# Performance work log

Hardware: AMD Instinct MI355X
Metric: run time of the kernel (lower is better)

Reference implementation:

```python
import jax, jax.numpy as jnp
import numpy as np
from jax import lax

SEQ = 8192
H = 2048
DEPTH = 2


def _rnn_layer(xs, h0, Wih, Whh, bih, bhh):
    """Elman RNN layer. xs: (T, B, F); h0: (B, H). Returns (hs (T,B,H), hT (B,H)).
    h_t = tanh(x_t @ Wih^T + b_ih + h_{t-1} @ Whh^T + b_hh)  (PyTorch nn.RNN math)."""
    # Precompute the input projection for all steps at once (one big GEMM).
    x_proj = jnp.einsum('tbf,hf->tbh', xs, Wih) + bih  # (T, B, H)

    def step(h, xp):
        h_new = jnp.tanh(xp + h @ Whh.T + bhh)
        return h_new, h_new

    hT, hs = lax.scan(step, h0, x_proj)
    return hs, hT


def setup_inputs() -> dict:
    key = jax.random.key(0)
    ks = jax.random.split(key, 10)
    s = 1.0 / np.sqrt(H)  # PyTorch nn.RNN init scale (uniform +-1/sqrt(H)); use scaled normal
    return {
        'x': jax.random.normal(ks[0], (1, SEQ), jnp.float32),
        'h': jax.random.normal(ks[1], (DEPTH, 1, H), jnp.float32),
        'W_ih_0': jax.random.normal(ks[2], (H, 1), jnp.float32) * s,
        'W_hh_0': jax.random.normal(ks[3], (H, H), jnp.float32) * s,
        'b_ih_0': jax.random.normal(ks[4], (H,), jnp.float32) * s,
        'b_hh_0': jax.random.normal(ks[5], (H,), jnp.float32) * s,
        'W_ih_1': jax.random.normal(ks[6], (H, H), jnp.float32) * s,
        'W_hh_1': jax.random.normal(ks[7], (H, H), jnp.float32) * s,
        'b_ih_1': jax.random.normal(ks[8], (H,), jnp.float32) * s,
        'b_hh_1': jax.random.normal(ks[9], (H,), jnp.float32) * s,
    }


def reference(x, h, W_ih_0, W_hh_0, b_ih_0, b_hh_0, W_ih_1, W_hh_1, b_ih_1, b_hh_1):
    # x: (1, SEQ) -> x.t()[..., None] -> (SEQ, 1, 1)
    xs = x.T[..., None]
    layers = [
        (W_ih_0, W_hh_0, b_ih_0, b_hh_0),
        (W_ih_1, W_hh_1, b_ih_1, b_hh_1),
    ]
    finals = []
    for l, (Wih, Whh, bih, bhh) in enumerate(layers):
        xs, hT = _rnn_layer(xs, h[l], Wih, Whh, bih, bhh)
        finals.append(hT)
    return jnp.stack(finals)  # (DEPTH, 1, H) == h_n from nn.RNN
```

## Files before the change

### kernel.cpp

```cpp
#include <hip/hip_runtime.h>
#include <hip/hip_bf16.h>

#define HD 2048
#define TT 8192
#define RPB 8
#define NTHR 256
#define SENTU 0xAAAAAAAAu


__device__ __forceinline__ float fix_sent(float v) {
    return (__float_as_uint(v) == SENTU) ? __uint_as_float(0xAAAAAABAu) : v;
}
__device__ __forceinline__ void slot_store(float* p, float v) {
    __hip_atomic_store(p, fix_sent(v), __ATOMIC_RELAXED, __HIP_MEMORY_SCOPE_AGENT);
}
__device__ __forceinline__ unsigned long long slot_load64(const unsigned long long* p) {
    return __hip_atomic_load(p, __ATOMIC_RELAXED, __HIP_MEMORY_SCOPE_AGENT);
}

__device__ __forceinline__ void poll8(const float* src, float* stash, long& gbudget) {
    const unsigned long long* p = reinterpret_cast<const unsigned long long*>(src);
    unsigned long long v[4];
    bool got[4] = {false, false, false, false};
    int passes = 1024;
    for (;;) {
        bool ok = true;
        #pragma unroll
        for (int j = 0; j < 4; ++j) if (!got[j]) {
            unsigned long long t = slot_load64(p + j);
            if ((unsigned)t != SENTU && (unsigned)(t >> 32) != SENTU) { v[j] = t; got[j] = true; }
            else ok = false;
        }
        if (ok) break;
        if (--passes < 0 || --gbudget < 0) {
            #pragma unroll
            for (int j = 0; j < 4; ++j) if (!got[j]) v[j] = 0ull;
            break;
        }
        if (passes < 1016) __builtin_amdgcn_s_sleep(1);
    }
    #pragma unroll
    for (int j = 0; j < 4; ++j) {
        stash[2*j]   = __uint_as_float((unsigned)v[j]);
        stash[2*j+1] = __uint_as_float((unsigned)(v[j] >> 32));
    }
}

__device__ __forceinline__ void poll8x2(const float* srcA, const float* srcB,
                                        float* stA, float* stB, long& gbudget) {
    const unsigned long long* pA = reinterpret_cast<const unsigned long long*>(srcA);
    const unsigned long long* pB = reinterpret_cast<const unsigned long long*>(srcB);
    unsigned long long vA[4], vB[4];
    bool gA[4] = {false,false,false,false}, gB[4] = {false,false,false,false};
    int passes = 1024;
    for (;;) {
        bool ok = true;
        #pragma unroll
        for (int j = 0; j < 4; ++j) {
            if (!gA[j]) {
                unsigned long long t = slot_load64(pA + j);
                if ((unsigned)t != SENTU && (unsigned)(t >> 32) != SENTU) { vA[j] = t; gA[j] = true; }
                else ok = false;
            }
            if (!gB[j]) {
                unsigned long long t = slot_load64(pB + j);
                if ((unsigned)t != SENTU && (unsigned)(t >> 32) != SENTU) { vB[j] = t; gB[j] = true; }
                else ok = false;
            }
        }
        if (ok) break;
        if (--passes < 0 || --gbudget < 0) {
            #pragma unroll
            for (int j = 0; j < 4; ++j) { if (!gA[j]) vA[j] = 0ull; if (!gB[j]) vB[j] = 0ull; }
            break;
        }
        if (passes < 1016) __builtin_amdgcn_s_sleep(1);
    }
    #pragma unroll
    for (int j = 0; j < 4; ++j) {
        stA[2*j]   = __uint_as_float((unsigned)vA[j]);
        stA[2*j+1] = __uint_as_float((unsigned)(vA[j] >> 32));
        stB[2*j]   = __uint_as_float((unsigned)vB[j]);
        stB[2*j+1] = __uint_as_float((unsigned)(vB[j] >> 32));
    }
}

__global__ __launch_bounds__(NTHR, 2)
void rnn_fused(const float* __restrict__ x,
               const float* __restrict__ h_init,
               const float* __restrict__ Wih0,
               const float* __restrict__ Whh0,
               const float* __restrict__ bih0,
               const float* __restrict__ bhh0,
               const float* __restrict__ Wih1,
               const float* __restrict__ Whh1,
               const float* __restrict__ bih1,
               const float* __restrict__ bhh1,
               float* __restrict__ slots0,
               float* __restrict__ slots1,
               float* __restrict__ out)
{
    __shared__ float hbA[2][HD];
    __shared__ float hbB[2][HD];

    const int tid = threadIdx.x;
    const int bid = blockIdx.x;
    const bool l0 = (bid < 256);
    const int rb  = l0 ? bid : (bid - 256);
    const int r   = tid >> 5;
    const int l   = tid & 31;
    const int row = rb * RPB + r;

    const int swz_w = ((tid >> 3) & 7) << 2;
    const int swz_r = (l & 7) << 2;

    float lastv = 0.f;
    long  gbudget = 1L << 21;

    if (l0) {
        float w[64];
        {
            const float4* wr = reinterpret_cast<const float4*>(Whh0 + (size_t)row * HD + l * 64);
            #pragma unroll
            for (int j = 0; j < 16; ++j) {
                float4 v = wr[j];
                w[4*j+0] = v.x; w[4*j+1] = v.y; w[4*j+2] = v.z; w[4*j+3] = v.w;
            }
        }
        const float wx   = Wih0[row];
        const float bias = bih0[row] + bhh0[row];

        if (l == 0) slot_store(&slots0[row], h_init[row]);

        for (int s = 0; s < TT; ++s) {
            float stash[8];
            poll8(slots0 + (size_t)s * HD + tid * 8, stash, gbudget);

            float* hbuf = hbA[s & 1];
            {
                const int base = tid * 8;
                float4 v0 = make_float4(stash[0], stash[1], stash[2], stash[3]);
                float4 v1 = make_float4(stash[4], stash[5], stash[6], stash[7]);
                *reinterpret_cast<float4*>(&hbuf[(base    ) ^ swz_w]) = v0;
                *reinterpret_cast<float4*>(&hbuf[(base + 4) ^ swz_w]) = v1;
            }
            __syncthreads();

            float acc = 0.f;
            const int hbase = l * 64;
            #pragma unroll
            for (int q = 0; q < 16; ++q) {
                float4 hv = *reinterpret_cast<const float4*>(&hbuf[(hbase + 4*q) ^ swz_r]);
                acc = fmaf(w[4*q+0], hv.x, acc);
                acc = fmaf(w[4*q+1], hv.y, acc);
                acc = fmaf(w[4*q+2], hv.z, acc);
                acc = fmaf(w[4*q+3], hv.w, acc);
            }
            #pragma unroll
            for (int m = 1; m < 32; m <<= 1) acc += __shfl_xor(acc, m);

            float val = tanhf(acc + bias + x[s] * wx);
            lastv = val;
            if (l == 0) slot_store(&slots0[(size_t)(s + 1) * HD + row], val);
        }
        if (l == 0) out[row] = lastv;
    } else {
        float wh[64], wi[64];
        {
            const float4* a = reinterpret_cast<const float4*>(Whh1 + (size_t)row * HD + l * 64);
            const float4* b = reinterpret_cast<const float4*>(Wih1 + (size_t)row * HD + l * 64);
            #pragma unroll
            for (int j = 0; j < 16; ++j) {
                float4 v = a[j];
                wh[4*j+0] = v.x; wh[4*j+1] = v.y; wh[4*j+2] = v.z; wh[4*j+3] = v.w;
                float4 u = b[j];
                wi[4*j+0] = u.x; wi[4*j+1] = u.y; wi[4*j+2] = u.z; wi[4*j+3] = u.w;
            }
        }
        const float bias = bih1[row] + bhh1[row];

        if (l == 0) slot_store(&slots1[row], h_init[HD + row]);

        for (int s = 0; s < TT; ++s) {
            float st1[8], st0[8];
            poll8x2(slots1 + (size_t)s * HD + tid * 8,
                    slots0 + (size_t)(s + 1) * HD + tid * 8,
                    st1, st0, gbudget);

            float* b1 = hbA[s & 1];
            float* b0 = hbB[s & 1];
            {
                const int base = tid * 8;
                *reinterpret_cast<float4*>(&b1[(base    ) ^ swz_w]) = make_float4(st1[0], st1[1], st1[2], st1[3]);
                *reinterpret_cast<float4*>(&b1[(base + 4) ^ swz_w]) = make_float4(st1[4], st1[5], st1[6], st1[7]);
                *reinterpret_cast<float4*>(&b0[(base    ) ^ swz_w]) = make_float4(st0[0], st0[1], st0[2], st0[3]);
                *reinterpret_cast<float4*>(&b0[(base + 4) ^ swz_w]) = make_float4(st0[4], st0[5], st0[6], st0[7]);
            }
            __syncthreads();

            float acc = 0.f;
            const int hbase = l * 64;
            #pragma unroll
            for (int q = 0; q < 16; ++q) {
                float4 h1v = *reinterpret_cast<const float4*>(&b1[(hbase + 4*q) ^ swz_r]);
                float4 h0v = *reinterpret_cast<const float4*>(&b0[(hbase + 4*q) ^ swz_r]);
                acc = fmaf(wh[4*q+0], h1v.x, acc);
                acc = fmaf(wh[4*q+1], h1v.y, acc);
                acc = fmaf(wh[4*q+2], h1v.z, acc);
                acc = fmaf(wh[4*q+3], h1v.w, acc);
                acc = fmaf(wi[4*q+0], h0v.x, acc);
                acc = fmaf(wi[4*q+1], h0v.y, acc);
                acc = fmaf(wi[4*q+2], h0v.z, acc);
                acc = fmaf(wi[4*q+3], h0v.w, acc);
            }
            #pragma unroll
            for (int m = 1; m < 32; m <<= 1) acc += __shfl_xor(acc, m);

            float val = tanhf(acc + bias);
            lastv = val;
            if (l == 0) slot_store(&slots1[(size_t)(s + 1) * HD + row], val);
        }
        if (l == 0) out[HD + row] = lastv;
    }
}

extern "C" void kernel_launch(void* const* d_in, const int* in_sizes, int n_in,
                              void* d_out, int out_size, void* d_ws, size_t ws_size,
                              hipStream_t stream)
{
    const float* x    = (const float*)d_in[0];
    const float* h    = (const float*)d_in[1];
    const float* Wih0 = (const float*)d_in[2];
    const float* Whh0 = (const float*)d_in[3];
    const float* bih0 = (const float*)d_in[4];
    const float* bhh0 = (const float*)d_in[5];
    const float* Wih1 = (const float*)d_in[6];
    const float* Whh1 = (const float*)d_in[7];
    const float* bih1 = (const float*)d_in[8];
    const float* bhh1 = (const float*)d_in[9];
    float* out = (float*)d_out;

    float* slots0 = (float*)d_ws;
    float* slots1 = slots0 + (size_t)(TT + 1) * HD;
    size_t need = (size_t)2 * (TT + 1) * HD * sizeof(float);
    if (ws_size < need) return;

    hipMemsetAsync(d_ws, 0xAA, need, stream);

    hipLaunchKernelGGL(rnn_fused, dim3(512), dim3(NTHR), 0, stream,
                       x, h, Wih0, Whh0, bih0, bhh0, Wih1, Whh1, bih1, bhh1,
                       slots0, slots1, out);
}
```

Measured before the change: 46.70 ms.

## Double rows per block, halve block count, and publish hidden state as paired 64-bit stores

Each block now handles 16 rows with 512 threads, so only 256 blocks (128 per layer) take part in the per-step spin-wait handoff instead of 512. Each wavefront packs its two rows' outputs into one 64-bit atomic store, and each thread polls 4 floats instead of 8. The x[s] load is hoisted ahead of the poll. The aim is to cut the number of producers and consumers and the store traffic in the per-timestep global handoff. In exchange, each block has fewer threads per row for polling, and with launch_bounds(512,2) holding 128 weight registers per thread, register pressure could limit occupancy.

Result: faster. 40.59 ms (-13.1%).

```diff
diff --git a/kernel.cpp b/kernel.cpp
--- a/kernel.cpp
+++ b/kernel.cpp
@@ -3,86 +3,62 @@
 
 #define HD 2048
 #define TT 8192
-#define RPB 8
-#define NTHR 256
+#define RPB 16
+#define NTHR 512
 #define SENTU 0xAAAAAAAAu
 
 
-__device__ __forceinline__ float fix_sent(float v) {
-    return (__float_as_uint(v) == SENTU) ? __uint_as_float(0xAAAAAABAu) : v;
-}
-__device__ __forceinline__ void slot_store(float* p, float v) {
-    __hip_atomic_store(p, fix_sent(v), __ATOMIC_RELAXED, __HIP_MEMORY_SCOPE_AGENT);
-}
-__device__ __forceinline__ unsigned long long slot_load64(const unsigned long long* p) {
+typedef unsigned long long ull;
+
+__device__ __forceinline__ unsigned fix_sent_u(float v) {
+    unsigned u = __float_as_uint(v);
+    return (u == SENTU) ? 0xAAAAAABAu : u;
+}
+__device__ __forceinline__ void slot_store_pair(ull* p, float lo, float hi) {
+    ull v = (ull)fix_sent_u(lo) | ((ull)fix_sent_u(hi) << 32);
+    __hip_atomic_store(p, v, __ATOMIC_RELAXED, __HIP_MEMORY_SCOPE_AGENT);
+}
+__device__ __forceinline__ ull slot_load64(const ull* p) {
     return __hip_atomic_load(p, __ATOMIC_RELAXED, __HIP_MEMORY_SCOPE_AGENT);
 }
-
-__device__ __forceinline__ void poll8(const float* src, float* stash, long& gbudget) {
-    const unsigned long long* p = reinterpret_cast<const unsigned long long*>(src);
-    unsigned long long v[4];
-    bool got[4] = {false, false, false, false};
+__device__ __forceinline__ bool pair_ok(ull t) {
+    return ((unsigned)t != SENTU) && ((unsigned)(t >> 32) != SENTU);
+}
+
+__device__ __forceinline__ void poll2(const ull* p, ull v[2], long& gb) {
+    bool g0 = false, g1 = false;
     int passes = 1024;
     for (;;) {
-        bool ok = true;
-        #pragma unroll
-        for (int j = 0; j < 4; ++j) if (!got[j]) {
-            unsigned long long t = slot_load64(p + j);
-            if ((unsigned)t != SENTU && (unsigned)(t >> 32) != SENTU) { v[j] = t; got[j] = true; }
-            else ok = false;
-        }
-        if (ok) break;
-        if (--passes < 0 || --gbudget < 0) {
-            #pragma unroll
-            for (int j = 0; j < 4; ++j) if (!got[j]) v[j] = 0ull;
-            break;
-        }
+        if (!g0) { ull t = slot_load64(p);     if (pair_ok(t)) { v[0] = t; g0 = true; } }
+        if (!g1) { ull t = slot_load64(p + 1); if (pair_ok(t)) { v[1] = t; g1 = true; } }
+        if (g0 && g1) return;
+        if (--passes < 0 || --gb < 0) { if (!g0) v[0] = 0; if (!g1) v[1] = 0; return; }
         if (passes < 1016) __builtin_amdgcn_s_sleep(1);
     }
-    #pragma unroll
-    for (int j = 0; j < 4; ++j) {
-        stash[2*j]   = __uint_as_float((unsigned)v[j]);
-        stash[2*j+1] = __uint_as_float((unsigned)(v[j] >> 32));
-    }
-}
-
-__device__ __forceinline__ void poll8x2(const float* srcA, const float* srcB,
-                                        float* stA, float* stB, long& gbudget) {
-    const unsigned long long* pA = reinterpret_cast<const unsigned long long*>(srcA);
-    const unsigned long long* pB = reinterpret_cast<const unsigned long long*>(srcB);
-    unsigned long long vA[4], vB[4];
-    bool gA[4] = {false,false,false,false}, gB[4] = {false,false,false,false};
+}
+__device__ __forceinline__ void poll2x2(const ull* pA, const ull* pB,
+                                        ull vA[2], ull vB[2], long& gb) {
+    bool a0=false, a1=false, b0=false, b1=false;
     int passes = 1024;
     for (;;) {
-        bool ok = true;
-        #pragma unroll
-        for (int j = 0; j < 4; ++j) {
-            if (!gA[j]) {
-                unsigned long long t = slot_load64(pA + j);
-                if ((unsigned)t != SENTU && (unsigned)(t >> 32) != SENTU) { vA[j] = t; gA[j] = true; }
-                else ok = false;
-            }
-            if (!gB[j]) {
-                unsigned long long t = slot_load64(pB + j);
-                if ((unsigned)t != SENTU && (unsigned)(t >> 32) != SENTU) { vB[j] = t; gB[j] = true; }
-                else ok = false;
-            }
-        }
-        if (ok) break;
-        if (--passes < 0 || --gbudget < 0) {
-            #pragma unroll
-            for (int j = 0; j < 4; ++j) { if (!gA[j]) vA[j] = 0ull; if (!gB[j]) vB[j] = 0ull; }
-            break;
+        if (!a0) { ull t = slot_load64(pA);     if (pair_ok(t)) { vA[0] = t; a0 = true; } }
+        if (!a1) { ull t = slot_load64(pA + 1); if (pair_ok(t)) { vA[1] = t; a1 = true; } }
+        if (!b0) { ull t = slot_load64(pB);     if (pair_ok(t)) { vB[0] = t; b0 = true; } }
+        if (!b1) { ull t = slot_load64(pB + 1); if (pair_ok(t)) { vB[1] = t; b1 = true; } }
+        if (a0 && a1 && b0 && b1) return;
+        if (--passes < 0 || --gb < 0) {
+            if (!a0) vA[0] = 0; if (!a1) vA[1] = 0;
+            if (!b0) vB[0] = 0; if (!b1) vB[1] = 0;
+            return;
         }
         if (passes < 1016) __builtin_amdgcn_s_sleep(1);
     }
-    #pragma unroll
-    for (int j = 0; j < 4; ++j) {
-        stA[2*j]   = __uint_as_float((unsigned)vA[j]);
-        stA[2*j+1] = __uint_as_float((unsigned)(vA[j] >> 32));
-        stB[2*j]   = __uint_as_float((unsigned)vB[j]);
-        stB[2*j+1] = __uint_as_float((unsigned)(vB[j] >> 32));
-    }
+}
+__device__ __forceinline__ float4 unpack4(ull v0, ull v1) {
+    return make_float4(__uint_as_float((unsigned)v0),
+                       __uint_as_float((unsigned)(v0 >> 32)),
+                       __uint_as_float((unsigned)v1),
+                       __uint_as_float((unsigned)(v1 >> 32)));
 }
 
 __global__ __launch_bounds__(NTHR, 2)
@@ -105,19 +81,23 @@
 
     const int tid = threadIdx.x;
     const int bid = blockIdx.x;
-    const bool l0 = (bid < 256);
-    const int rb  = l0 ? bid : (bid - 256);
+    const bool is_l0 = (bid < 128);
+    const int blk = is_l0 ? bid : (bid - 128);
     const int r   = tid >> 5;
     const int l   = tid & 31;
-    const int row = rb * RPB + r;
-
-    const int swz_w = ((tid >> 3) & 7) << 2;
+    const int fl  = tid & 63;
+    const int wid = tid >> 6;
+    const int row = blk * RPB + r;
+
+    const int swz_w = ((tid >> 4) & 7) << 2;
     const int swz_r = (l & 7) << 2;
+
+    const size_t mypair_w = (size_t)blk * RPB + 2 * wid;
 
     float lastv = 0.f;
     long  gbudget = 1L << 21;
 
-    if (l0) {
+    if (is_l0) {
         float w[64];
         {
             const float4* wr = reinterpret_cast<const float4*>(Whh0 + (size_t)row * HD + l * 64);
@@ -130,22 +110,22 @@
         const float wx   = Wih0[row];
         const float bias = bih0[row] + bhh0[row];
 
-        if (l == 0) slot_store(&slots0[row], h_init[row]);
+        {
+            float v0 = h_init[row];
+            float v1 = __shfl_xor(v0, 32);
+            if (fl == 0)
+                slot_store_pair(reinterpret_cast<ull*>(slots0 + mypair_w), v0, v1);
+        }
 
         for (int s = 0; s < TT; ++s) {
-            float stash[8];
-            poll8(slots0 + (size_t)s * HD + tid * 8, stash, gbudget);
-
-            float* hbuf = hbA[s & 1];
-            {
-                const int base = tid * 8;
-                float4 v0 = make_float4(stash[0], stash[1], stash[2], stash[3]);
-                float4 v1 = make_float4(stash[4], stash[5], stash[6], stash[7]);
-                *reinterpret_cast<float4*>(&hbuf[(base    ) ^ swz_w]) = v0;
-                *reinterpret_cast<float4*>(&hbuf[(base + 4) ^ swz_w]) = v1;
-            }
+            const float xv = x[s];
+            ull pv[2];
+            poll2(reinterpret_cast<const ull*>(slots0 + (size_t)s * HD + tid * 4), pv, gbudget);
+
+            *reinterpret_cast<float4*>(&hbA[s & 1][(tid * 4) ^ swz_w]) = unpack4(pv[0], pv[1]);
             __syncthreads();
 
+            const float* hbuf = hbA[s & 1];
             float acc = 0.f;
             const int hbase = l * 64;
             #pragma unroll
@@ -159,9 +139,12 @@
             #pragma unroll
             for (int m = 1; m < 32; m <<= 1) acc += __shfl_xor(acc, m);
 
-            float val = tanhf(acc + bias + x[s] * wx);
+            float val = tanhf(acc + bias + xv * wx);
             lastv = val;
-            if (l == 0) slot_store(&slots0[(size_t)(s + 1) * HD + row], val);
+            float v1 = __shfl_xor(val, 32);
+            if (fl == 0)
+                slot_store_pair(reinterpret_cast<ull*>(slots0 + (size_t)(s + 1) * HD + mypair_w),
+                                val, v1);
         }
         if (l == 0) out[row] = lastv;
     } else {
@@ -179,25 +162,25 @@
         }
         const float bias = bih1[row] + bhh1[row];
 
-        if (l == 0) slot_store(&slots1[row], h_init[HD + row]);
+        {
+            float v0 = h_init[HD + row];
+            float v1 = __shfl_xor(v0, 32);
+            if (fl == 0)
+                slot_store_pair(reinterpret_cast<ull*>(slots1 + mypair_w), v0, v1);
+        }
 
         for (int s = 0; s < TT; ++s) {
-            float st1[8], st0[8];
-            poll8x2(slots1 + (size_t)s * HD + tid * 8,
-                    slots0 + (size_t)(s + 1) * HD + tid * 8,
-                    st1, st0, gbudget);
-
-            float* b1 = hbA[s & 1];
-            float* b0 = hbB[s & 1];
-            {
-                const int base = tid * 8;
-                *reinterpret_cast<float4*>(&b1[(base    ) ^ swz_w]) = make_float4(st1[0], st1[1], st1[2], st1[3]);
-                *reinterpret_cast<float4*>(&b1[(base + 4) ^ swz_w]) = make_float4(st1[4], st1[5], st1[6], st1[7]);
-                *reinterpret_cast<float4*>(&b0[(base    ) ^ swz_w]) = make_float4(st0[0], st0[1], st0[2], st0[3]);
-                *reinterpret_cast<float4*>(&b0[(base + 4) ^ swz_w]) = make_float4(st0[4], st0[5], st0[6], st0[7]);
-            }
+            ull p1[2], p0[2];
+            poll2x2(reinterpret_cast<const ull*>(slots1 + (size_t)s * HD + tid * 4),
+                    reinterpret_cast<const ull*>(slots0 + (size_t)(s + 1) * HD + tid * 4),
+                    p1, p0, gbudget);
+
+            *reinterpret_cast<float4*>(&hbA[s & 1][(tid * 4) ^ swz_w]) = unpack4(p1[0], p1[1]);
+            *reinterpret_cast<float4*>(&hbB[s & 1][(tid * 4) ^ swz_w]) = unpack4(p0[0], p0[1]);
             __syncthreads();
 
+            const float* b1 = hbA[s & 1];
+            const float* b0 = hbB[s & 1];
             float acc = 0.f;
             const int hbase = l * 64;
             #pragma unroll
@@ -218,7 +201,10 @@
 
             float val = tanhf(acc + bias);
             lastv = val;
-            if (l == 0) slot_store(&slots1[(size_t)(s + 1) * HD + row], val);
+            float v1 = __shfl_xor(val, 32);
+            if (fl == 0)
+                slot_store_pair(reinterpret_cast<ull*>(slots1 + (size_t)(s + 1) * HD + mypair_w),
+                                val, v1);
         }
         if (l == 0) out[HD + row] = lastv;
     }
@@ -247,7 +233,7 @@
 
     hipMemsetAsync(d_ws, 0xAA, need, stream);
 
-    hipLaunchKernelGGL(rnn_fused, dim3(512), dim3(NTHR), 0, stream,
+    hipLaunchKernelGGL(rnn_fused, dim3(256), dim3(NTHR), 0, stream,
                        x, h, Wih0, Whh0, bih0, bhh0, Wih1, Whh1, bih1, bhh1,
                        slots0, slots1, out);
 }
```
